# Kernel optimization log

Hardware: AMD Instinct MI355X
Metric: run time of the kernel (lower is better)

Reference implementation:

```python
import jax, jax.numpy as jnp
import numpy as np

B, E, H, W, P, C = 2, 256, 192, 192, 16, 80
GRIDS = (40, 36, 24, 16, 12)
L = len(GRIDS)
MASK_W, CLS_W, ALPHA, GAMMA, EPS = 3.0, 1.0, 0.25, 2.0, 1e-4


def setup_inputs() -> dict:
    key = jax.random.key(0)
    ks = jax.random.split(key, 32)
    inp = {"mask_out": jax.random.normal(ks[0], (B, E, H, W), jnp.float32)}
    for i, g in enumerate(GRIDS):
        inp[f"kernel_l{i}"] = jax.random.normal(ks[1 + i], (B, g, g, E), jnp.float32) * 0.05
        inp[f"cate_l{i}"] = jax.random.uniform(ks[6 + i], (B, g, g, C), jnp.float32)
        inp[f"pos_l{i}"] = jax.random.randint(ks[11 + i], (B, P), 0, g * g, dtype=jnp.int32)
        inp[f"cate_t_l{i}"] = jax.random.randint(ks[16 + i], (B, g, g), -1, C, dtype=jnp.int32)
    # binary instance masks, image-major layout [B, L, P, H, W]
    inp["mask_targets"] = (jax.random.uniform(ks[21], (B, L, P, H, W)) > 0.9).astype(jnp.float32)
    return inp


def _forward(mask_out, kernels, cates, mask_targets, pos_idxs, cate_ts):
    # --- dynamic 1x1 conv: gather positive kernels and apply as batched matmul ---
    preds = []
    for kl, pl in zip(kernels, pos_idxs):
        g2 = kl.shape[1] * kl.shape[2]
        kflat = kl.reshape(B, g2, E)
        kp = jnp.take_along_axis(kflat, pl[:, :, None], axis=1)  # [B, P, E]
        preds.append(jnp.einsum('bpe,behw->bphw', kp, mask_out))  # F.conv2d 1x1
    preds = jnp.stack(preds)  # [L, B, P, H, W]  (level-major, matches torch cat order)

    # --- dice loss ---
    mp = jax.nn.sigmoid(preds).reshape(L * B * P, H * W)
    # NOTE: original code concatenates targets image-major (img, level) while preds
    # are level-major (level, img); we reproduce that pairing faithfully.
    mt = mask_targets.reshape(B * L * P, H * W)
    a = jnp.sum(mp * mt, axis=1)
    b = jnp.sum(mp * mp, axis=1)
    c = jnp.sum(mt * mt, axis=1)
    mask_loss = jnp.sum(1.0 - 2.0 * a / (b + c + 1e-4)) / (L * B * P)

    # --- focal loss on positive grid cells ---
    tgt = jnp.concatenate([t.reshape(-1) for t in cate_ts])            # [N]
    prd = jnp.concatenate([cl.reshape(-1, C) for cl in cates])          # [N, C]
    posm = (tgt > -1).astype(jnp.float32)
    p = jnp.clip(prd, EPS, 1.0 - EPS)
    gt = jax.nn.one_hot(jnp.clip(tgt, 0, C - 1), C, dtype=jnp.float32)
    af = jnp.where(gt == 1.0, ALPHA, 1.0 - ALPHA)
    pt = jnp.where(gt == 1.0, p, 1.0 - p)
    fw = af * (1.0 - pt) ** GAMMA
    ce = -(gt * jnp.log(p) + (1.0 - gt) * jnp.log(1.0 - p))
    cls_loss = jnp.sum(fw * ce * posm[:, None]) / jnp.sum(posm)

    return jnp.stack([MASK_W * mask_loss, CLS_W * cls_loss])  # [mask_loss, cls_loss]


def reference(mask_out, kernel_l0, kernel_l1, kernel_l2, kernel_l3, kernel_l4,
              cate_l0, cate_l1, cate_l2, cate_l3, cate_l4, mask_targets,
              pos_l0, pos_l1, pos_l2, pos_l3, pos_l4,
              cate_t_l0, cate_t_l1, cate_t_l2, cate_t_l3, cate_t_l4):
    return _forward(mask_out,
                    (kernel_l0, kernel_l1, kernel_l2, kernel_l3, kernel_l4),
                    (cate_l0, cate_l1, cate_l2, cate_l3, cate_l4),
                    mask_targets,
                    (pos_l0, pos_l1, pos_l2, pos_l3, pos_l4),
                    (cate_t_l0, cate_t_l1, cate_t_l2, cate_t_l3, cate_t_l4))
```

## Files before the change

kernel.cpp:

```cpp
#include <hip/hip_runtime.h>
#include <hip/hip_bf16.h>

namespace {

constexpr int kHW = 36864;
constexpr int kFocalElems = 7744 * 80;

typedef __attribute__((ext_vector_type(8))) short bf16x8;
typedef __attribute__((ext_vector_type(4))) float f32x4;

__device__ __forceinline__ unsigned short f2bf(float x) {
  return __builtin_bit_cast(unsigned short, __float2bfloat16(x));
}

__device__ __forceinline__ float wave_sum(float v) {
#pragma unroll
  for (int off = 32; off; off >>= 1) v += __shfl_xor(v, off, 64);
  return v;
}

__global__ __launch_bounds__(128) void gather_k(
    const float* __restrict__ k0, const float* __restrict__ k1,
    const float* __restrict__ k2, const float* __restrict__ k3,
    const float* __restrict__ k4,
    const int* __restrict__ q0, const int* __restrict__ q1,
    const int* __restrict__ q2, const int* __restrict__ q3,
    const int* __restrict__ q4,
    unsigned short* __restrict__ kbf) {
  const int b = blockIdx.y;
  const int row = blockIdx.x;
  const int l = row >> 4, p = row & 15;
  const float* kb[5] = {k0, k1, k2, k3, k4};
  const int* pb[5] = {q0, q1, q2, q3, q4};
  const int bg2[5] = {b * 1600, b * 1296, b * 576, b * 256, b * 144};
  const int pos = pb[l][b * 16 + p];
  const int ch = threadIdx.x * 2;
  const float2 kv = *(const float2*)(kb[l] + (size_t)(bg2[l] + pos) * 256 + ch);
  *(unsigned int*)&kbf[((size_t)b * 80 + row) * 256 + ch] =
      (unsigned int)f2bf(kv.x) | ((unsigned int)f2bf(kv.y) << 16);
}

__global__ __launch_bounds__(256, 4) void solov2_main(
    const float* __restrict__ mask_out,
    const unsigned short* __restrict__ kbf,
    const float* __restrict__ mask_targets,
    float* __restrict__ acc) {
  const int b = blockIdx.y;
  const int lane = threadIdx.x & 63;
  const int wv = threadIdx.x >> 6;
  const int px16 = lane & 15;
  const int hi8 = (lane >> 4) * 8;
  const int pxl = blockIdx.x * 64 + wv * 16 + px16;

  const float* __restrict__ mop =
      mask_out + (size_t)b * 256 * kHW + (size_t)hi8 * kHW + pxl;
  const unsigned short* __restrict__ ka =
      kbf + ((size_t)b * 80 + px16) * 256 + hi8;

  __shared__ float bred[4][240];

  f32x4 a5[5];
#pragma unroll
  for (int mt = 0; mt < 5; ++mt) a5[mt] = (f32x4){0.f, 0.f, 0.f, 0.f};

  float pf0[8], pf1[8], pf2[8];

#define PF(BUF, KS)                                                         \
  {                                                                         \
    _Pragma("unroll") for (int j = 0; j < 8; ++j)                           \
        BUF[j] = mop[(size_t)((KS) * 32 + j) * kHW];                        \
  }

#define STEP(BUF, KS)                                                       \
  {                                                                         \
    bf16x8 bb;                                                              \
    _Pragma("unroll") for (int j = 0; j < 8; ++j)                           \
        bb[j] = (short)f2bf(BUF[j]);                                        \
    _Pragma("unroll") for (int mt = 0; mt < 5; ++mt) {                      \
      const bf16x8 af = *(const bf16x8*)(ka + mt * 4096 + (KS) * 32);       \
      a5[mt] = __builtin_amdgcn_mfma_f32_16x16x32_bf16(af, bb, a5[mt],      \
                                                       0, 0, 0);            \
    }                                                                       \
  }

  PF(pf0, 0);
  PF(pf1, 1);
  PF(pf2, 2); STEP(pf0, 0);
  PF(pf0, 3); STEP(pf1, 1);
  PF(pf1, 4); STEP(pf2, 2);
  PF(pf2, 5); STEP(pf0, 3);
  PF(pf0, 6); STEP(pf1, 4);
  PF(pf1, 7); STEP(pf2, 5);
  STEP(pf0, 6);
  STEP(pf1, 7);
#undef PF
#undef STEP

#pragma unroll
  for (int mt = 0; mt < 5; ++mt) {
#pragma unroll
    for (int j = 0; j < 4; ++j) {
      const int row80 = mt * 16 + (lane >> 4) * 4 + j;
      const int r = (row80 >> 4) * 32 + b * 16 + (row80 & 15);
      const float x0 = a5[mt][j];
      const float mp = 1.f / (1.f + __expf(-x0));
      const float tv = mask_targets[(size_t)r * kHW + pxl];
      float av = mp * tv;
      float bv = mp * mp;
      float cv = tv;
#pragma unroll
      for (int m = 1; m <= 8; m <<= 1) {
        av += __shfl_xor(av, m, 64);
        bv += __shfl_xor(bv, m, 64);
        cv += __shfl_xor(cv, m, 64);
      }
      if (px16 == 0) {
        bred[wv][row80] = av;
        bred[wv][80 + row80] = bv;
        bred[wv][160 + row80] = cv;
      }
    }
  }
  __syncthreads();
  if (threadIdx.x < 240) {
    const int q = threadIdx.x / 80;
    const int row80 = threadIdx.x - q * 80;
    const int r = (row80 >> 4) * 32 + b * 16 + (row80 & 15);
    const float s = bred[0][threadIdx.x] + bred[1][threadIdx.x] +
                    bred[2][threadIdx.x] + bred[3][threadIdx.x];
    unsafeAtomicAdd(&acc[q * 160 + r], s);
  }
}

__global__ __launch_bounds__(256) void focal_kernel(
    const float* __restrict__ c0, const float* __restrict__ c1,
    const float* __restrict__ c2, const float* __restrict__ c3,
    const float* __restrict__ c4,
    const int* __restrict__ t0, const int* __restrict__ t1,
    const int* __restrict__ t2, const int* __restrict__ t3,
    const int* __restrict__ t4,
    float* __restrict__ acc) {
  float term = 0.f, np = 0.f;
  for (int idx = blockIdx.x * 256 + threadIdx.x; idx < kFocalElems;
       idx += gridDim.x * 256) {
    const int n = idx / 80;
    const int c = idx - n * 80;
    int t;
    const float* crow;
    if (n < 3200) {
      t = t0[n]; crow = c0 + (size_t)n * 80;
    } else if (n < 5792) {
      const int o = n - 3200; t = t1[o]; crow = c1 + (size_t)o * 80;
    } else if (n < 6944) {
      const int o = n - 5792; t = t2[o]; crow = c2 + (size_t)o * 80;
    } else if (n < 7456) {
      const int o = n - 6944; t = t3[o]; crow = c3 + (size_t)o * 80;
    } else {
      const int o = n - 7456; t = t4[o]; crow = c4 + (size_t)o * 80;
    }
    if (t > -1) {
      float pv = crow[c];
      pv = fminf(fmaxf(pv, 1e-4f), 1.f - 1e-4f);
      const bool gm = (c == t);
      const float af = gm ? 0.25f : 0.75f;
      const float pt = gm ? pv : 1.f - pv;
      const float om = 1.f - pt;
      term = fmaf(af * om * om, -__logf(pt), term);
      if (c == 0) np += 1.f;
    }
  }
  term = wave_sum(term);
  np = wave_sum(np);
  __shared__ float st[8];
  const int wid = threadIdx.x >> 6;
  if ((threadIdx.x & 63) == 0) {
    st[wid] = term;
    st[4 + wid] = np;
  }
  __syncthreads();
  if (threadIdx.x == 0) {
    unsafeAtomicAdd(&acc[480], st[0] + st[1] + st[2] + st[3]);
    unsafeAtomicAdd(&acc[481], st[4] + st[5] + st[6] + st[7]);
  }
}

__global__ void zero_kernel(float* __restrict__ acc) {
  const int i = blockIdx.x * 256 + threadIdx.x;
  if (i < 482) acc[i] = 0.f;
}

__global__ __launch_bounds__(64) void finalize_kernel(
    const float* __restrict__ acc, float* __restrict__ out) {
  const int tid = threadIdx.x;
  float s = 0.f;
#pragma unroll
  for (int rr = 0; rr < 3; ++rr) {
    const int r = tid + rr * 64;
    if (r < 160) {
      const float a = acc[r];
      const float bb = acc[160 + r];
      const float cc = acc[320 + r];
      s += 1.f - 2.f * a / (bb + cc + 1e-4f);
    }
  }
  s = wave_sum(s);
  if (tid == 0) {
    out[0] = 3.0f * (s / 160.f);
    out[1] = acc[480] / acc[481];
  }
}

}

extern "C" void kernel_launch(void* const* d_in, const int* in_sizes, int n_in,
                              void* d_out, int out_size, void* d_ws,
                              size_t ws_size, hipStream_t stream) {
  const float* mask_out = (const float*)d_in[0];
  const float* k[5];
  const float* cc[5];
  const int* pp[5];
  const int* tt[5];
  for (int i = 0; i < 5; ++i) {
    k[i] = (const float*)d_in[1 + 4 * i];
    cc[i] = (const float*)d_in[2 + 4 * i];
    pp[i] = (const int*)d_in[3 + 4 * i];
    tt[i] = (const int*)d_in[4 + 4 * i];
  }
  const float* mt = (const float*)d_in[21];
  float* acc = (float*)d_ws;
  unsigned short* kbf = (unsigned short*)((float*)d_ws + 512);
  float* out = (float*)d_out;

  hipLaunchKernelGGL(zero_kernel, dim3(2), dim3(256), 0, stream, acc);
  hipLaunchKernelGGL(gather_k, dim3(80, 2), dim3(128), 0, stream,
                     k[0], k[1], k[2], k[3], k[4], pp[0], pp[1], pp[2], pp[3],
                     pp[4], kbf);
  hipLaunchKernelGGL(solov2_main, dim3(576, 2), dim3(256), 0, stream,
                     mask_out, kbf, mt, acc);
  hipLaunchKernelGGL(focal_kernel, dim3(320), dim3(256), 0, stream, cc[0],
                     cc[1], cc[2], cc[3], cc[4], tt[0], tt[1], tt[2], tt[3],
                     tt[4], acc);
  hipLaunchKernelGGL(finalize_kernel, dim3(1), dim3(64), 0, stream, acc, out);
}
```

Baseline: 73.93 us.

## Stage mask_out through LDS with async global_load_lds double buffering; vectorize focal loss

The main kernel stops doing strided per-lane register prefetches of mask_out. Instead it loads 16-byte chunks straight into a double-buffered LDS tile with global_load_lds, and each k-step reads operands from LDS before the MFMA, with a barrier per step. Occupancy hint is lowered to 2 blocks per CU to fit the extra shared memory. Separately, the focal kernel now uses one thread per 4 classes with float4 loads and a grid that exactly covers the elements, replacing the grid-stride loop. The price is a barrier each k-step and possibly less latency hiding from lower occupancy.

```diff
diff --git a/kernel.cpp b/kernel.cpp
--- a/kernel.cpp
+++ b/kernel.cpp
@@ -4,7 +4,7 @@
 namespace {
 
 constexpr int kHW = 36864;
-constexpr int kFocalElems = 7744 * 80;
+constexpr int kFocalQuads = 7744 * 20;
 
 typedef __attribute__((ext_vector_type(8))) short bf16x8;
 typedef __attribute__((ext_vector_type(4))) float f32x4;
@@ -40,7 +40,7 @@
       (unsigned int)f2bf(kv.x) | ((unsigned int)f2bf(kv.y) << 16);
 }
 
-__global__ __launch_bounds__(256, 4) void solov2_main(
+__global__ __launch_bounds__(256, 2) void solov2_main(
     const float* __restrict__ mask_out,
     const unsigned short* __restrict__ kbf,
     const float* __restrict__ mask_targets,
@@ -50,51 +50,60 @@
   const int wv = threadIdx.x >> 6;
   const int px16 = lane & 15;
   const int hi8 = (lane >> 4) * 8;
-  const int pxl = blockIdx.x * 64 + wv * 16 + px16;
-
-  const float* __restrict__ mop =
-      mask_out + (size_t)b * 256 * kHW + (size_t)hi8 * kHW + pxl;
+  const int px0 = blockIdx.x * 64;
+  const int pxl = px0 + wv * 16 + px16;
+
+  __shared__ float bufB[2][32][64];
+  __shared__ float bred[4][240];
+
   const unsigned short* __restrict__ ka =
       kbf + ((size_t)b * 80 + px16) * 256 + hi8;
 
-  __shared__ float bred[4][240];
+  const float* __restrict__ gstage = mask_out + (size_t)b * 256 * kHW +
+                                     (size_t)(wv * 4 + (lane >> 4)) * kHW +
+                                     px0 + (lane & 15) * 4;
+
+#define STAGE(CUR, KS)                                                       \
+  {                                                                          \
+    const float* gs = gstage + (size_t)(KS)*32 * kHW;                        \
+    __builtin_amdgcn_global_load_lds(                                        \
+        (const __attribute__((address_space(1))) unsigned int*)gs,           \
+        (__attribute__((address_space(3))) unsigned int*)&bufB[CUR][wv * 4]  \
+            [0],                                                             \
+        16, 0, 0);                                                           \
+    __builtin_amdgcn_global_load_lds(                                        \
+        (const __attribute__((address_space(1))) unsigned int*)(gs +         \
+                                                                16 * kHW),   \
+        (__attribute__((address_space(3))) unsigned int*)&bufB[CUR][wv * 4 + \
+                                                                   16][0],   \
+        16, 0, 0);                                                           \
+  }
 
   f32x4 a5[5];
 #pragma unroll
   for (int mt = 0; mt < 5; ++mt) a5[mt] = (f32x4){0.f, 0.f, 0.f, 0.f};
 
-  float pf0[8], pf1[8], pf2[8];
-
-#define PF(BUF, KS)                                                         \
-  {                                                                         \
-    _Pragma("unroll") for (int j = 0; j < 8; ++j)                           \
-        BUF[j] = mop[(size_t)((KS) * 32 + j) * kHW];                        \
-  }
-
-#define STEP(BUF, KS)                                                       \
-  {                                                                         \
-    bf16x8 bb;                                                              \
-    _Pragma("unroll") for (int j = 0; j < 8; ++j)                           \
-        bb[j] = (short)f2bf(BUF[j]);                                        \
-    _Pragma("unroll") for (int mt = 0; mt < 5; ++mt) {                      \
-      const bf16x8 af = *(const bf16x8*)(ka + mt * 4096 + (KS) * 32);       \
-      a5[mt] = __builtin_amdgcn_mfma_f32_16x16x32_bf16(af, bb, a5[mt],      \
-                                                       0, 0, 0);            \
-    }                                                                       \
-  }
-
-  PF(pf0, 0);
-  PF(pf1, 1);
-  PF(pf2, 2); STEP(pf0, 0);
-  PF(pf0, 3); STEP(pf1, 1);
-  PF(pf1, 4); STEP(pf2, 2);
-  PF(pf2, 5); STEP(pf0, 3);
-  PF(pf0, 6); STEP(pf1, 4);
-  PF(pf1, 7); STEP(pf2, 5);
-  STEP(pf0, 6);
-  STEP(pf1, 7);
-#undef PF
-#undef STEP
+  STAGE(0, 0);
+  __syncthreads();
+
+#pragma unroll
+  for (int ks = 0; ks < 8; ++ks) {
+    if (ks + 1 < 8) STAGE((ks + 1) & 1, ks + 1);
+    float fb[8];
+#pragma unroll
+    for (int j = 0; j < 8; ++j) fb[j] = bufB[ks & 1][hi8 + j][wv * 16 + px16];
+    bf16x8 bb;
+#pragma unroll
+    for (int j = 0; j < 8; ++j) bb[j] = (short)f2bf(fb[j]);
+#pragma unroll
+    for (int mt = 0; mt < 5; ++mt) {
+      const bf16x8 af = *(const bf16x8*)(ka + mt * 4096 + ks * 32);
+      a5[mt] =
+          __builtin_amdgcn_mfma_f32_16x16x32_bf16(af, bb, a5[mt], 0, 0, 0);
+    }
+    __syncthreads();
+  }
+#undef STAGE
 
 #pragma unroll
   for (int mt = 0; mt < 5; ++mt) {
@@ -140,34 +149,36 @@
     const int* __restrict__ t2, const int* __restrict__ t3,
     const int* __restrict__ t4,
     float* __restrict__ acc) {
+  const int idx = blockIdx.x * 256 + threadIdx.x;
+  const int n = idx / 20;
+  const int cq = (idx - n * 20) * 4;
+  int t;
+  const float* crow;
+  if (n < 3200) {
+    t = t0[n]; crow = c0 + (size_t)n * 80;
+  } else if (n < 5792) {
+    const int o = n - 3200; t = t1[o]; crow = c1 + (size_t)o * 80;
+  } else if (n < 6944) {
+    const int o = n - 5792; t = t2[o]; crow = c2 + (size_t)o * 80;
+  } else if (n < 7456) {
+    const int o = n - 6944; t = t3[o]; crow = c3 + (size_t)o * 80;
+  } else {
+    const int o = n - 7456; t = t4[o]; crow = c4 + (size_t)o * 80;
+  }
   float term = 0.f, np = 0.f;
-  for (int idx = blockIdx.x * 256 + threadIdx.x; idx < kFocalElems;
-       idx += gridDim.x * 256) {
-    const int n = idx / 80;
-    const int c = idx - n * 80;
-    int t;
-    const float* crow;
-    if (n < 3200) {
-      t = t0[n]; crow = c0 + (size_t)n * 80;
-    } else if (n < 5792) {
-      const int o = n - 3200; t = t1[o]; crow = c1 + (size_t)o * 80;
-    } else if (n < 6944) {
-      const int o = n - 5792; t = t2[o]; crow = c2 + (size_t)o * 80;
-    } else if (n < 7456) {
-      const int o = n - 6944; t = t3[o]; crow = c3 + (size_t)o * 80;
-    } else {
-      const int o = n - 7456; t = t4[o]; crow = c4 + (size_t)o * 80;
-    }
-    if (t > -1) {
-      float pv = crow[c];
-      pv = fminf(fmaxf(pv, 1e-4f), 1.f - 1e-4f);
-      const bool gm = (c == t);
+  if (t > -1) {
+    const float4 pv4 = *(const float4*)&crow[cq];
+    const float pvs[4] = {pv4.x, pv4.y, pv4.z, pv4.w};
+#pragma unroll
+    for (int j = 0; j < 4; ++j) {
+      float pv = fminf(fmaxf(pvs[j], 1e-4f), 1.f - 1e-4f);
+      const bool gm = (cq + j == t);
       const float af = gm ? 0.25f : 0.75f;
       const float pt = gm ? pv : 1.f - pv;
       const float om = 1.f - pt;
       term = fmaf(af * om * om, -__logf(pt), term);
-      if (c == 0) np += 1.f;
-    }
+    }
+    if (cq == 0) np = 1.f;
   }
   term = wave_sum(term);
   np = wave_sum(np);
@@ -232,12 +243,11 @@
   float* out = (float*)d_out;
 
   hipLaunchKernelGGL(zero_kernel, dim3(2), dim3(256), 0, stream, acc);
-  hipLaunchKernelGGL(gather_k, dim3(80, 2), dim3(128), 0, stream,
-                     k[0], k[1], k[2], k[3], k[4], pp[0], pp[1], pp[2], pp[3],
-                     pp[4], kbf);
-  hipLaunchKernelGGL(solov2_main, dim3(576, 2), dim3(256), 0, stream,
-                     mask_out, kbf, mt, acc);
-  hipLaunchKernelGGL(focal_kernel, dim3(320), dim3(256), 0, stream, cc[0],
+  hipLaunchKernelGGL(gather_k, dim3(80, 2), dim3(128), 0, stream, k[0], k[1],
+                     k[2], k[3], k[4], pp[0], pp[1], pp[2], pp[3], pp[4], kbf);
+  hipLaunchKernelGGL(solov2_main, dim3(576, 2), dim3(256), 0, stream, mask_out,
+                     kbf, mt, acc);
+  hipLaunchKernelGGL(focal_kernel, dim3(605), dim3(256), 0, stream, cc[0],
                      cc[1], cc[2], cc[3], cc[4], tt[0], tt[1], tt[2], tt[3],
                      tt[4], acc);
   hipLaunchKernelGGL(finalize_kernel, dim3(1), dim3(64), 0, stream, acc, out);
```

Measured after the change: 78.26 us. 5.9% more time.
